# Kernel tuning notes

Hardware: AMD Instinct MI355X
Metric: run time of the kernel (lower is better)

Reference implementation:

```python
import jax, jax.numpy as jnp
import numpy as np


def setup_inputs() -> dict:
    key = jax.random.key(0)
    k1, k2 = jax.random.split(key)
    B, M, L, C, F, K = 8, 32, 1024, 256, 256, 3
    x = jax.random.normal(k1, (B, M, L, C), dtype=jnp.float32)
    W = jax.random.normal(k2, (K, C, F), dtype=jnp.float32) * 0.02  # WIO layout
    b = jnp.zeros((F,), dtype=jnp.float32)
    return {"x": x, "W": W, "b": b}


def reference(x, W, b):
    # Original: tf.map_fn(Conv1D, x) over leading axis of [B, M, L, C].
    # Mathematically identical to one batched 'valid' Conv1D on [B*M, L, C].
    B, M, L, C = x.shape
    K, _, F = W.shape
    xf = x.reshape(B * M, L, C)
    y = jax.lax.conv_general_dilated(
        xf, W,
        window_strides=(1,),
        padding='VALID',
        dimension_numbers=('NWC', 'WIO', 'NWC'),
    ) + b
    return y.reshape(B, M, L - K + 1, F)
```

## Files before the change

kernel.cpp:

```cpp
#include <hip/hip_runtime.h>

typedef __attribute__((ext_vector_type(8))) short short8;
typedef __attribute__((ext_vector_type(4))) float f32x4;

constexpr int L = 1024, C = 256, F = 256;
constexpr int NIMG = 256;
constexpr int LOUT = 1022;
constexpr long MAXROW = (long)NIMG * L - 1;

__device__ inline unsigned short f2bf(float f) {
  union { float f; unsigned u; } v; v.f = f;
  return (unsigned short)((v.u + 0x7FFFu + ((v.u >> 16) & 1u)) >> 16);
}

__device__ inline void g2l16(const unsigned short* g, unsigned short* l) {
  __builtin_amdgcn_global_load_lds(
      (const __attribute__((address_space(1))) unsigned int*)g,
      (__attribute__((address_space(3))) unsigned int*)l, 16, 0, 0);
}

__global__ void wprep(const float* __restrict__ W, unsigned short* __restrict__ Wt) {
  int tid = blockIdx.x * 256 + threadIdx.x;
  int kc = tid >> 8, f = tid & 255;
  int k = kc >> 8, c = kc & 255;
  int slab = c >> 5, kp = c & 31;
  int fh = f >> 7, fp = f & 127;
  Wt[(size_t)((((slab * 3 + k) * 2 + fh) * 128 + fp) * 32 + kp)] = f2bf(W[tid]);
}

__global__ __launch_bounds__(256) void conv_mfma(
    const float* __restrict__ x, const unsigned short* __restrict__ Wt,
    const float* __restrict__ bias, float* __restrict__ y)
{
  __shared__ __align__(16) unsigned short As[2][130 * 32];
  __shared__ __align__(16) unsigned short Bs[3][128 * 32];

  const int bid = blockIdx.x;
  const int fh  = bid & 1;
  const int mt  = (bid >> 1) & 7;
  const int img = bid >> 4;
  const int l0  = mt * 128;

  const int tid  = threadIdx.x;
  const int lane = tid & 63;
  const int wv   = tid >> 6;
  const int wr   = wv >> 1;
  const int wc   = wv & 1;
  const int lr   = lane & 15;
  const int quad = lane >> 4;

  f32x4 acc[4][4] = {};
  float4 av[2][2];
  float4 avt[2];

  const long gb  = (long)img * L + l0;
  const int  qr  = tid >> 2;
  const int  qc8 = (tid & 3) * 8;

  auto issue_A = [&](int slab) {
    const int cb = slab * 32;
    long g0 = gb + qr;        if (g0 > MAXROW) g0 = MAXROW;
    long g1 = gb + qr + 64;   if (g1 > MAXROW) g1 = MAXROW;
    const float* p0 = x + g0 * C + cb + qc8;
    const float* p1 = x + g1 * C + cb + qc8;
    av[0][0] = *(const float4*)p0; av[0][1] = *(const float4*)(p0 + 4);
    av[1][0] = *(const float4*)p1; av[1][1] = *(const float4*)(p1 + 4);
    if (tid < 8) {
      long g2 = gb + 128 + (tid >> 2); if (g2 > MAXROW) g2 = MAXROW;
      const float* p2 = x + g2 * C + cb + (tid & 3) * 8;
      avt[0] = *(const float4*)p2; avt[1] = *(const float4*)(p2 + 4);
    }
  };

  auto pack8 = [&](float4 a, float4 b) {
    short8 r;
    r[0] = (short)f2bf(a.x); r[1] = (short)f2bf(a.y);
    r[2] = (short)f2bf(a.z); r[3] = (short)f2bf(a.w);
    r[4] = (short)f2bf(b.x); r[5] = (short)f2bf(b.y);
    r[6] = (short)f2bf(b.z); r[7] = (short)f2bf(b.w);
    return r;
  };

  auto write_A = [&](int ab) {
    *(short8*)(As[ab] + (size_t)tid * 8)         = pack8(av[0][0], av[0][1]);
    *(short8*)(As[ab] + (size_t)(tid + 256) * 8) = pack8(av[1][0], av[1][1]);
    if (tid < 8)
      *(short8*)(As[ab] + (size_t)(512 + tid) * 8) = pack8(avt[0], avt[1]);
  };

  auto stage_B = [&](int tile, int bb) {
    const unsigned short* bsrc = Wt + (size_t)(tile * 2 + fh) * 4096;
    g2l16(bsrc + (size_t)tid * 8,         Bs[bb] + (size_t)tid * 8);
    g2l16(bsrc + (size_t)(tid + 256) * 8, Bs[bb] + (size_t)(tid + 256) * 8);
  };

  issue_A(0);
  stage_B(0, 0);
  stage_B(1, 1);
  write_A(0);
  asm volatile("s_waitcnt vmcnt(2) lgkmcnt(0)" ::: "memory");
  __builtin_amdgcn_s_barrier();
  __builtin_amdgcn_sched_barrier(0);

  for (int slab = 0; slab < 8; ++slab) {
    const int ab = slab & 1;
#pragma unroll
    for (int k = 0; k < 3; ++k) {
      if (slab < 7 || k == 0)
        stage_B(slab * 3 + k + 2, (k + 2) % 3);
      if (k == 0 && slab < 7) issue_A(slab + 1);

      short8 af[4], bf[4];
#pragma unroll
      for (int mi = 0; mi < 4; ++mi)
        af[mi] = *(const short8*)(As[ab] + (wr * 64 + mi * 16 + lr + k) * 32 + quad * 8);
#pragma unroll
      for (int ni = 0; ni < 4; ++ni)
        bf[ni] = *(const short8*)(Bs[k] + (wc * 64 + ni * 16 + lr) * 32 + quad * 8);

      if (k == 2 && slab < 7) write_A(ab ^ 1);

      __builtin_amdgcn_s_setprio(1);
#pragma unroll
      for (int mi = 0; mi < 4; ++mi)
#pragma unroll
        for (int ni = 0; ni < 4; ++ni)
          acc[mi][ni] = __builtin_amdgcn_mfma_f32_16x16x32_bf16(af[mi], bf[ni], acc[mi][ni], 0, 0, 0);
      __builtin_amdgcn_s_setprio(0);

      if (slab * 3 + k < 23) {
        if (slab < 7) {
          if (k < 2) asm volatile("s_waitcnt vmcnt(6)" ::: "memory");
          else       asm volatile("s_waitcnt vmcnt(2) lgkmcnt(0)" ::: "memory");
        } else {
          if (k == 0) asm volatile("s_waitcnt vmcnt(2)" ::: "memory");
          else        asm volatile("s_waitcnt vmcnt(0)" ::: "memory");
        }
        __builtin_amdgcn_s_barrier();
        __builtin_amdgcn_sched_barrier(0);
      }
    }
  }

  float bv[4];
#pragma unroll
  for (int ni = 0; ni < 4; ++ni)
    bv[ni] = bias[fh * 128 + wc * 64 + ni * 16 + lr];

#pragma unroll
  for (int mi = 0; mi < 4; ++mi) {
#pragma unroll
    for (int r = 0; r < 4; ++r) {
      const int lrow = l0 + wr * 64 + mi * 16 + quad * 4 + r;
      if (lrow < LOUT) {
        float* yp = y + ((size_t)img * LOUT + lrow) * F + fh * 128 + wc * 64 + lr;
#pragma unroll
        for (int ni = 0; ni < 4; ++ni)
          yp[ni * 16] = acc[mi][ni][r] + bv[ni];
      }
    }
  }
}

extern "C" void kernel_launch(void* const* d_in, const int* in_sizes, int n_in,
                              void* d_out, int out_size, void* d_ws, size_t ws_size,
                              hipStream_t stream) {
  const float* x = (const float*)d_in[0];
  const float* W = (const float*)d_in[1];
  const float* b = (const float*)d_in[2];
  float* y = (float*)d_out;
  unsigned short* Wt = (unsigned short*)d_ws;

  wprep<<<768, 256, 0, stream>>>(W, Wt);
  conv_mfma<<<NIMG * 8 * 2, 256, 0, stream>>>(x, Wt, b, y);
}
```

Before: 513.6 us.

## Cover all 256 output channels per block with 8 waves to halve input reads

Each workgroup now computes a 128x256 output tile with 512 threads (2x4 waves), where before it was 128x128 with 256 threads. The x input slab is therefore loaded and converted to bf16 once rather than twice, halving global input traffic and conversion work. The weight layout is flattened to match, and the barrier/waitcnt schedule is restructured so the wait and barrier come at the top of each step and the A write is moved after the MFMAs. In exchange, LDS use per block and the block size go up, and there are half as many blocks.

After: 469.2 us. 8.6% less time.

```diff
diff --git a/kernel.cpp b/kernel.cpp
--- a/kernel.cpp
+++ b/kernel.cpp
@@ -24,47 +24,40 @@
   int kc = tid >> 8, f = tid & 255;
   int k = kc >> 8, c = kc & 255;
   int slab = c >> 5, kp = c & 31;
-  int fh = f >> 7, fp = f & 127;
-  Wt[(size_t)((((slab * 3 + k) * 2 + fh) * 128 + fp) * 32 + kp)] = f2bf(W[tid]);
+  Wt[(size_t)(((slab * 3 + k) * 256 + f) * 32 + kp)] = f2bf(W[tid]);
 }
 
-__global__ __launch_bounds__(256) void conv_mfma(
+__global__ __launch_bounds__(512, 4) void conv_mfma(
     const float* __restrict__ x, const unsigned short* __restrict__ Wt,
     const float* __restrict__ bias, float* __restrict__ y)
 {
-  __shared__ __align__(16) unsigned short As[2][130 * 32];
-  __shared__ __align__(16) unsigned short Bs[3][128 * 32];
+  __shared__ __align__(16) unsigned short As[2][520 * 8];
+  __shared__ __align__(16) unsigned short Bs[3][512 * 16];
 
   const int bid = blockIdx.x;
-  const int fh  = bid & 1;
-  const int mt  = (bid >> 1) & 7;
-  const int img = bid >> 4;
+  const int mt  = bid & 7;
+  const int img = bid >> 3;
   const int l0  = mt * 128;
 
   const int tid  = threadIdx.x;
   const int lane = tid & 63;
   const int wv   = tid >> 6;
-  const int wr   = wv >> 1;
-  const int wc   = wv & 1;
+  const int wr   = wv >> 2;
+  const int wc   = wv & 3;
   const int lr   = lane & 15;
   const int quad = lane >> 4;
 
   f32x4 acc[4][4] = {};
-  float4 av[2][2];
+  float4 av[2];
   float4 avt[2];
 
-  const long gb  = (long)img * L + l0;
-  const int  qr  = tid >> 2;
-  const int  qc8 = (tid & 3) * 8;
+  const long gb = (long)img * L + l0;
 
   auto issue_A = [&](int slab) {
     const int cb = slab * 32;
-    long g0 = gb + qr;        if (g0 > MAXROW) g0 = MAXROW;
-    long g1 = gb + qr + 64;   if (g1 > MAXROW) g1 = MAXROW;
-    const float* p0 = x + g0 * C + cb + qc8;
-    const float* p1 = x + g1 * C + cb + qc8;
-    av[0][0] = *(const float4*)p0; av[0][1] = *(const float4*)(p0 + 4);
-    av[1][0] = *(const float4*)p1; av[1][1] = *(const float4*)(p1 + 4);
+    long g0 = gb + (tid >> 2); if (g0 > MAXROW) g0 = MAXROW;
+    const float* p0 = x + g0 * C + cb + (tid & 3) * 8;
+    av[0] = *(const float4*)p0; av[1] = *(const float4*)(p0 + 4);
     if (tid < 8) {
       long g2 = gb + 128 + (tid >> 2); if (g2 > MAXROW) g2 = MAXROW;
       const float* p2 = x + g2 * C + cb + (tid & 3) * 8;
@@ -81,33 +74,40 @@
     return r;
   };
 
-  auto write_A = [&](int ab) {
-    *(short8*)(As[ab] + (size_t)tid * 8)         = pack8(av[0][0], av[0][1]);
-    *(short8*)(As[ab] + (size_t)(tid + 256) * 8) = pack8(av[1][0], av[1][1]);
+  auto write_A = [&](int ab2) {
+    *(short8*)(As[ab2] + (size_t)tid * 8) = pack8(av[0], av[1]);
     if (tid < 8)
-      *(short8*)(As[ab] + (size_t)(512 + tid) * 8) = pack8(avt[0], avt[1]);
+      *(short8*)(As[ab2] + (size_t)(512 + tid) * 8) = pack8(avt[0], avt[1]);
   };
 
   auto stage_B = [&](int tile, int bb) {
-    const unsigned short* bsrc = Wt + (size_t)(tile * 2 + fh) * 4096;
+    const unsigned short* bsrc = Wt + (size_t)tile * 8192;
     g2l16(bsrc + (size_t)tid * 8,         Bs[bb] + (size_t)tid * 8);
-    g2l16(bsrc + (size_t)(tid + 256) * 8, Bs[bb] + (size_t)(tid + 256) * 8);
+    g2l16(bsrc + (size_t)(tid + 512) * 8, Bs[bb] + (size_t)(tid + 512) * 8);
   };
 
   issue_A(0);
   stage_B(0, 0);
   stage_B(1, 1);
   write_A(0);
-  asm volatile("s_waitcnt vmcnt(2) lgkmcnt(0)" ::: "memory");
-  __builtin_amdgcn_s_barrier();
-  __builtin_amdgcn_sched_barrier(0);
 
   for (int slab = 0; slab < 8; ++slab) {
     const int ab = slab & 1;
 #pragma unroll
     for (int k = 0; k < 3; ++k) {
-      if (slab < 7 || k == 0)
-        stage_B(slab * 3 + k + 2, (k + 2) % 3);
+      if (slab < 7) {
+        if (k == 0)      asm volatile("s_waitcnt vmcnt(2) lgkmcnt(0)" ::: "memory");
+        else             asm volatile("s_waitcnt vmcnt(4)" ::: "memory");
+      } else {
+        if (k == 0)      asm volatile("s_waitcnt vmcnt(2) lgkmcnt(0)" ::: "memory");
+        else if (k == 1) asm volatile("s_waitcnt vmcnt(2)" ::: "memory");
+        else             asm volatile("s_waitcnt vmcnt(0)" ::: "memory");
+      }
+      __builtin_amdgcn_s_barrier();
+      __builtin_amdgcn_sched_barrier(0);
+
+      const int t = slab * 3 + k;
+      if (t < 22) stage_B(t + 2, (k + 2) % 3);
       if (k == 0 && slab < 7) issue_A(slab + 1);
 
       short8 af[4], bf[4];
@@ -118,8 +118,6 @@
       for (int ni = 0; ni < 4; ++ni)
         bf[ni] = *(const short8*)(Bs[k] + (wc * 64 + ni * 16 + lr) * 32 + quad * 8);
 
-      if (k == 2 && slab < 7) write_A(ab ^ 1);
-
       __builtin_amdgcn_s_setprio(1);
 #pragma unroll
       for (int mi = 0; mi < 4; ++mi)
@@ -128,24 +126,14 @@
           acc[mi][ni] = __builtin_amdgcn_mfma_f32_16x16x32_bf16(af[mi], bf[ni], acc[mi][ni], 0, 0, 0);
       __builtin_amdgcn_s_setprio(0);
 
-      if (slab * 3 + k < 23) {
-        if (slab < 7) {
-          if (k < 2) asm volatile("s_waitcnt vmcnt(6)" ::: "memory");
-          else       asm volatile("s_waitcnt vmcnt(2) lgkmcnt(0)" ::: "memory");
-        } else {
-          if (k == 0) asm volatile("s_waitcnt vmcnt(2)" ::: "memory");
-          else        asm volatile("s_waitcnt vmcnt(0)" ::: "memory");
-        }
-        __builtin_amdgcn_s_barrier();
-        __builtin_amdgcn_sched_barrier(0);
-      }
+      if (k == 2 && slab < 7) write_A(ab ^ 1);
     }
   }
 
   float bv[4];
 #pragma unroll
   for (int ni = 0; ni < 4; ++ni)
-    bv[ni] = bias[fh * 128 + wc * 64 + ni * 16 + lr];
+    bv[ni] = bias[wc * 64 + ni * 16 + lr];
 
 #pragma unroll
   for (int mi = 0; mi < 4; ++mi) {
@@ -153,7 +141,7 @@
     for (int r = 0; r < 4; ++r) {
       const int lrow = l0 + wr * 64 + mi * 16 + quad * 4 + r;
       if (lrow < LOUT) {
-        float* yp = y + ((size_t)img * LOUT + lrow) * F + fh * 128 + wc * 64 + lr;
+        float* yp = y + ((size_t)img * LOUT + lrow) * F + wc * 64 + lr;
 #pragma unroll
         for (int ni = 0; ni < 4; ++ni)
           yp[ni * 16] = acc[mi][ni][r] + bv[ni];
@@ -172,5 +160,5 @@
   unsigned short* Wt = (unsigned short*)d_ws;
 
   wprep<<<768, 256, 0, stream>>>(W, Wt);
-  conv_mfma<<<NIMG * 8 * 2, 256, 0, stream>>>(x, Wt, b, y);
+  conv_mfma<<<NIMG * 8, 512, 0, stream>>>(x, Wt, b, y);
 }
```
